# Performance work log

Hardware: AMD Instinct MI355X
Metric: run time of the kernel (lower is better)

Reference implementation:

```python
import jax, jax.numpy as jnp
import numpy as np

EMBED_DIM = 1024
NUM_HEADS = 16
HEAD_DIM = EMBED_DIM // NUM_HEADS
BATCH = 2
SEQ = 2048


def setup_inputs() -> dict:
    key = jax.random.key(0)
    ks = jax.random.split(key, 9)
    s = 1.0 / np.sqrt(EMBED_DIM)
    x = jax.random.normal(ks[0], (BATCH, SEQ, EMBED_DIM), dtype=jnp.float32)
    Wq = jax.random.uniform(ks[1], (EMBED_DIM, EMBED_DIM), jnp.float32, -s, s)
    bq = jax.random.uniform(ks[2], (EMBED_DIM,), jnp.float32, -s, s)
    Wk = jax.random.uniform(ks[3], (EMBED_DIM, EMBED_DIM), jnp.float32, -s, s)
    bk = jax.random.uniform(ks[4], (EMBED_DIM,), jnp.float32, -s, s)
    Wv = jax.random.uniform(ks[5], (EMBED_DIM, EMBED_DIM), jnp.float32, -s, s)
    bv = jax.random.uniform(ks[6], (EMBED_DIM,), jnp.float32, -s, s)
    Wo = jax.random.uniform(ks[7], (EMBED_DIM, EMBED_DIM), jnp.float32, -s, s)
    bo = jax.random.uniform(ks[8], (EMBED_DIM,), jnp.float32, -s, s)
    return {"x": x, "Wq": Wq, "bq": bq, "Wk": Wk, "bk": bk,
            "Wv": Wv, "bv": bv, "Wo": Wo, "bo": bo}


def reference(x, Wq, bq, Wk, bk, Wv, bv, Wo, bo):
    B, S, E = x.shape
    H, D = NUM_HEADS, HEAD_DIM

    def split_heads(t):
        # [B, S, E] -> [B, H, S, D]
        return t.reshape(B, S, H, D).transpose(0, 2, 1, 3)

    q = split_heads(x @ Wq + bq)
    k = split_heads(x @ Wk + bk)
    v = split_heads(x @ Wv + bv)

    scale = 1.0 / np.sqrt(D).astype(np.float32)
    scores = jnp.einsum('bhqd,bhkd->bhqk', q, k) * scale  # [B,H,S,S]
    attn = jax.nn.softmax(scores, axis=-1)
    out = jnp.einsum('bhqk,bhkd->bhqd', attn, v)  # [B,H,S,D]
    out = out.transpose(0, 2, 1, 3).reshape(B, S, E)
    return out @ Wo + bo
```

## Files before the change

### kernel.cpp

```cpp
#include <hip/hip_runtime.h>
#include <cstdint>

#define BATCH 2
#define SEQ   2048
#define EMB   1024
#define NHEAD 16
#define HDIM  64
#define NTOK  (BATCH*SEQ)

typedef __attribute__((ext_vector_type(8))) short bf16x8;
typedef __attribute__((ext_vector_type(8))) short short8;
typedef __attribute__((ext_vector_type(4))) float f32x4;

__device__ inline unsigned short f2bf(float f) {
    unsigned u = __float_as_uint(f);
    u += 0x7FFF + ((u >> 16) & 1);
    return (unsigned short)(u >> 16);
}

__device__ inline unsigned cvt_pk_bf16(float lo, float hi) {
    unsigned r;
    asm("v_cvt_pk_bf16_f32 %0, %1, %2" : "=v"(r) : "v"(lo), "v"(hi));
    return r;
}

__device__ inline void gload16(const void* g, void* lds) {
    __builtin_amdgcn_global_load_lds(
        (const __attribute__((address_space(1))) unsigned int*)g,
        (__attribute__((address_space(3))) unsigned int*)lds, 16, 0, 0);
}

__global__ __launch_bounds__(256)
void conv_x(const float* __restrict__ x, unsigned short* __restrict__ xb) {
    int i = (blockIdx.x * 256 + threadIdx.x) * 8;
    float4 a = *(const float4*)(x + i);
    float4 b = *(const float4*)(x + i + 4);
    short8 o;
    o[0]=f2bf(a.x); o[1]=f2bf(a.y); o[2]=f2bf(a.z); o[3]=f2bf(a.w);
    o[4]=f2bf(b.x); o[5]=f2bf(b.y); o[6]=f2bf(b.z); o[7]=f2bf(b.w);
    *(short8*)(xb + i) = o;
}

__global__ __launch_bounds__(256)
void conv_wt(const float* __restrict__ Wq, const float* __restrict__ Wk,
             const float* __restrict__ Wv, const float* __restrict__ Wo,
             unsigned short* __restrict__ Wt) {
    const float* W = blockIdx.z==0?Wq : blockIdx.z==1?Wk : blockIdx.z==2?Wv : Wo;
    unsigned short* out = Wt + (size_t)blockIdx.z * EMB * EMB;
    __shared__ float T[64][68];
    const int t = threadIdx.x;
    const int k0 = blockIdx.x * 64, n0 = blockIdx.y * 64;
    #pragma unroll
    for (int rr = 0; rr < 4; ++rr) {
        int row = (t >> 4) + 16 * rr;
        float4 v = *(const float4*)(W + (size_t)(k0+row)*EMB + n0 + (t&15)*4);
        *(float4*)&T[row][(t&15)*4] = v;
    }
    __syncthreads();
    #pragma unroll
    for (int it = 0; it < 2; ++it) {
        int ci = it*256 + t;
        int nr = ci >> 3, kc = ci & 7;
        short8 o;
        #pragma unroll
        for (int j = 0; j < 8; ++j) o[j] = f2bf(T[kc*8+j][nr]);
        *(short8*)(out + (size_t)(n0+nr)*EMB + k0 + kc*8) = o;
    }
}

__global__ __launch_bounds__(256)
void gemm_qkv(const unsigned short* __restrict__ xb, const unsigned short* __restrict__ Wt,
              const float* __restrict__ bq, const float* __restrict__ bk,
              const float* __restrict__ bv,
              unsigned short* __restrict__ Qb, unsigned short* __restrict__ Kb,
              unsigned short* __restrict__ Vb) {
    const int z = blockIdx.z;
    const unsigned short* W = Wt + (size_t)z * EMB * EMB;
    const float* bias = z==0 ? bq : z==1 ? bk : bv;
    unsigned short* out = z==0 ? Qb : z==1 ? Kb : Vb;
    const float scale = z==0 ? 0.125f : 1.0f;

    __shared__ __align__(16) unsigned short As[128*32];
    __shared__ __align__(16) unsigned short Bs[128*32];

    const int tid = threadIdx.x, lane = tid & 63, wid = tid >> 6;
    const int m0 = blockIdx.y * 128, n0 = blockIdx.x * 128;
    const int wr = wid >> 1, wc = wid & 1;

    f32x4 acc[4][4];
    #pragma unroll
    for (int i = 0; i < 4; ++i)
        #pragma unroll
        for (int j = 0; j < 4; ++j) acc[i][j] = f32x4{0.f,0.f,0.f,0.f};

    for (int k0 = 0; k0 < EMB; k0 += 32) {
        #pragma unroll
        for (int it = 0; it < 2; ++it) {
            int cbase = it*256 + wid*64;
            int ci = cbase + lane;
            int row = ci >> 2;
            int c = (ci & 3) ^ ((row >> 1) & 3);
            gload16(xb + (size_t)(m0+row)*EMB + k0 + c*8, (char*)As + cbase*16);
            gload16(W  + (size_t)(n0+row)*EMB + k0 + c*8, (char*)Bs + cbase*16);
        }
        __syncthreads();
        bf16x8 af[4], bf[4];
        #pragma unroll
        for (int i = 0; i < 4; ++i) {
            int ar = 64*wr + 16*i + (lane & 15);
            int ac = (lane >> 4) ^ ((ar >> 1) & 3);
            af[i] = *(const bf16x8*)((const char*)As + ar*64 + ac*16);
            int br = 64*wc + 16*i + (lane & 15);
            int bc = (lane >> 4) ^ ((br >> 1) & 3);
            bf[i] = *(const bf16x8*)((const char*)Bs + br*64 + bc*16);
        }
        #pragma unroll
        for (int i = 0; i < 4; ++i)
            #pragma unroll
            for (int j = 0; j < 4; ++j)
                acc[i][j] = __builtin_amdgcn_mfma_f32_16x16x32_bf16(af[i], bf[j], acc[i][j], 0, 0, 0);
        __syncthreads();
    }

    #pragma unroll
    for (int j = 0; j < 4; ++j) {
        int col = n0 + 64*wc + 16*j + (lane & 15);
        float bvv = bias[col];
        #pragma unroll
        for (int i = 0; i < 4; ++i) {
            int row0 = m0 + 64*wr + 16*i + (lane >> 4) * 4;
            #pragma unroll
            for (int r = 0; r < 4; ++r)
                out[(size_t)(row0+r)*EMB + col] = f2bf((acc[i][j][r] + bvv) * scale);
        }
    }
}

__global__ __launch_bounds__(256)
void gemm_out(const unsigned short* __restrict__ Cb, const unsigned short* __restrict__ Wto,
              const float* __restrict__ bo, float* __restrict__ out) {
    __shared__ __align__(16) unsigned short As[128*32];
    __shared__ __align__(16) unsigned short Bs[128*32];

    const int tid = threadIdx.x, lane = tid & 63, wid = tid >> 6;
    const int m0 = blockIdx.y * 128, n0 = blockIdx.x * 128;
    const int wr = wid >> 1, wc = wid & 1;

    f32x4 acc[4][4];
    #pragma unroll
    for (int i = 0; i < 4; ++i)
        #pragma unroll
        for (int j = 0; j < 4; ++j) acc[i][j] = f32x4{0.f,0.f,0.f,0.f};

    for (int k0 = 0; k0 < EMB; k0 += 32) {
        #pragma unroll
        for (int it = 0; it < 2; ++it) {
            int cbase = it*256 + wid*64;
            int ci = cbase + lane;
            int row = ci >> 2;
            int c = (ci & 3) ^ ((row >> 1) & 3);
            gload16(Cb  + (size_t)(m0+row)*EMB + k0 + c*8, (char*)As + cbase*16);
            gload16(Wto + (size_t)(n0+row)*EMB + k0 + c*8, (char*)Bs + cbase*16);
        }
        __syncthreads();
        bf16x8 af[4], bf[4];
        #pragma unroll
        for (int i = 0; i < 4; ++i) {
            int ar = 64*wr + 16*i + (lane & 15);
            int ac = (lane >> 4) ^ ((ar >> 1) & 3);
            af[i] = *(const bf16x8*)((const char*)As + ar*64 + ac*16);
            int br = 64*wc + 16*i + (lane & 15);
            int bc = (lane >> 4) ^ ((br >> 1) & 3);
            bf[i] = *(const bf16x8*)((const char*)Bs + br*64 + bc*16);
        }
        #pragma unroll
        for (int i = 0; i < 4; ++i)
            #pragma unroll
            for (int j = 0; j < 4; ++j)
                acc[i][j] = __builtin_amdgcn_mfma_f32_16x16x32_bf16(af[i], bf[j], acc[i][j], 0, 0, 0);
        __syncthreads();
    }

    #pragma unroll
    for (int j = 0; j < 4; ++j) {
        int col = n0 + 64*wc + 16*j + (lane & 15);
        float bvv = bo[col];
        #pragma unroll
        for (int i = 0; i < 4; ++i) {
            int row0 = m0 + 64*wr + 16*i + (lane >> 4) * 4;
            #pragma unroll
            for (int r = 0; r < 4; ++r)
                out[(size_t)(row0+r)*EMB + col] = acc[i][j][r] + bvv;
        }
    }
}

__global__ __launch_bounds__(256, 4)
void attn(const unsigned short* __restrict__ Qg, const unsigned short* __restrict__ Kg,
          const unsigned short* __restrict__ Vg, unsigned short* __restrict__ Cg) {
    __shared__ __align__(16) unsigned short Ks[2][64*64];
    __shared__ __align__(16) unsigned short Vs[2][64*64];

    const int tid = threadIdx.x, lane = tid & 63, wid = tid >> 6;
    const int qb = blockIdx.x, bh = blockIdx.y;
    const int b = bh >> 4, h = bh & 15;
    const size_t base = (size_t)b * SEQ * EMB + (size_t)h * HDIM;
    const unsigned short* Qp = Qg + base + (size_t)qb * 64 * EMB;
    const unsigned short* Kp = Kg + base;
    const unsigned short* Vp = Vg + base;

    #pragma unroll
    for (int it = 0; it < 2; ++it) {
        int ci = it*256 + tid, row = ci >> 3, c = (ci & 7) ^ (row & 7);
        gload16(Qp + (size_t)row*EMB + c*8, (char*)Ks[0] + (it*256 + wid*64)*16);
    }
    __syncthreads();
    bf16x8 qf[2];
    #pragma unroll
    for (int kc = 0; kc < 2; ++kc) {
        int r = 16*wid + (lane & 15);
        int c = ((lane >> 4) + 4*kc) ^ (r & 7);
        qf[kc] = *(const bf16x8*)((const char*)Ks[0] + r*128 + c*16);
    }
    __syncthreads();

    const int vc = tid & 7;
    const int vp = tid >> 3;

    #pragma unroll
    for (int it = 0; it < 2; ++it) {
        int ci = it*256 + tid, row = ci >> 3, c = (ci & 7) ^ (row & 7);
        gload16(Kp + (size_t)row*EMB + c*8, (char*)Ks[0] + (it*256 + wid*64)*16);
    }
    {
        short8 v0 = *(const short8*)(Vp + (size_t)(2*vp)*EMB + vc*8);
        short8 v1 = *(const short8*)(Vp + (size_t)(2*vp+1)*EMB + vc*8);
        unsigned* dst = (unsigned*)Vs[0];
        #pragma unroll
        for (int i = 0; i < 8; ++i) {
            int d = vc*8 + i;
            unsigned u = ((unsigned)(unsigned short)v1[i] << 16) | (unsigned short)v0[i];
            int slot = (vp >> 2) ^ (d & 7) ^ ((d >> 3) & 7);
            dst[d*32 + slot*4 + (vp & 3)] = u;
        }
    }
    __syncthreads();

    f32x4 O[4];
    #pragma unroll
    for (int j = 0; j < 4; ++j) O[j] = f32x4{0.f,0.f,0.f,0.f};
    float m_run = -3.0e38f, l_run = 0.f;
    const float L2E = 1.44269504f;

    for (int kt = 0; kt < SEQ/64; ++kt) {
        const int cur = kt & 1, nxt = cur ^ 1;
        short8 w0, w1;
        if (kt < SEQ/64 - 1) {
            const unsigned short* Kt = Kp + (size_t)(kt+1)*64*EMB;
            const unsigned short* Vt = Vp + (size_t)(kt+1)*64*EMB;
            #pragma unroll
            for (int it = 0; it < 2; ++it) {
                int ci = it*256 + tid, row = ci >> 3, c = (ci & 7) ^ (row & 7);
                gload16(Kt + (size_t)row*EMB + c*8, (char*)Ks[nxt] + (it*256 + wid*64)*16);
            }
            w0 = *(const short8*)(Vt + (size_t)(2*vp)*EMB + vc*8);
            w1 = *(const short8*)(Vt + (size_t)(2*vp+1)*EMB + vc*8);
        }

        f32x4 s[4];
        #pragma unroll
        for (int nk = 0; nk < 4; ++nk) {
            s[nk] = f32x4{0.f,0.f,0.f,0.f};
            #pragma unroll
            for (int kc = 0; kc < 2; ++kc) {
                int r = 16*nk + (lane & 15);
                int c = ((lane >> 4) + 4*kc) ^ (r & 7);
                bf16x8 kf = *(const bf16x8*)((const char*)Ks[cur] + r*128 + c*16);
                s[nk] = __builtin_amdgcn_mfma_f32_16x16x32_bf16(kf, qf[kc], s[nk], 0, 0, 0);
            }
        }

        float mx = s[0][0];
        #pragma unroll
        for (int nk = 0; nk < 4; ++nk)
            #pragma unroll
            for (int r = 0; r < 4; ++r) mx = fmaxf(mx, s[nk][r]);
        mx = fmaxf(mx, __shfl_xor(mx, 16));
        mx = fmaxf(mx, __shfl_xor(mx, 32));

        if (!__all(mx <= m_run + 8.0f)) {
            float mn = fmaxf(m_run, mx);
            float al = exp2f((m_run - mn) * L2E);
            m_run = mn;
            l_run *= al;
            float ar[4];
            #pragma unroll
            for (int r = 0; r < 4; ++r) ar[r] = __shfl(al, (lane >> 4)*4 + r);
            #pragma unroll
            for (int jd = 0; jd < 4; ++jd)
                #pragma unroll
                for (int r = 0; r < 4; ++r) O[jd][r] *= ar[r];
        }
        float msc = m_run * L2E;
        float ps = 0.f;
        #pragma unroll
        for (int nk = 0; nk < 4; ++nk)
            #pragma unroll
            for (int r = 0; r < 4; ++r) {
                float p = exp2f(fmaf(s[nk][r], L2E, -msc));
                s[nk][r] = p;
                ps += p;
            }
        ps += __shfl_xor(ps, 16);
        ps += __shfl_xor(ps, 32);
        l_run += ps;

        unsigned pk[4][2];
        #pragma unroll
        for (int nk = 0; nk < 4; ++nk) {
            pk[nk][0] = cvt_pk_bf16(s[nk][0], s[nk][1]);
            pk[nk][1] = cvt_pk_bf16(s[nk][2], s[nk][3]);
        }
        const int hh = lane >> 4;
        const int srcA = (((hh << 1) & 3) << 4) | (lane & 15);
        const int srcB = srcA + 16;
        const int hs = hh >> 1;
        bf16x8 pf[2];
        #pragma unroll
        for (int kc = 0; kc < 2; ++kc) {
            union { unsigned u[4]; bf16x8 v; } cvt;
            unsigned a0 = __shfl((int)pk[2*kc][0], srcA), b0 = __shfl((int)pk[2*kc+1][0], srcA);
            cvt.u[0] = hs ? b0 : a0;
            unsigned a1 = __shfl((int)pk[2*kc][1], srcA), b1 = __shfl((int)pk[2*kc+1][1], srcA);
            cvt.u[1] = hs ? b1 : a1;
            unsigned a2 = __shfl((int)pk[2*kc][0], srcB), b2 = __shfl((int)pk[2*kc+1][0], srcB);
            cvt.u[2] = hs ? b2 : a2;
            unsigned a3 = __shfl((int)pk[2*kc][1], srcB), b3 = __shfl((int)pk[2*kc+1][1], srcB);
            cvt.u[3] = hs ? b3 : a3;
            pf[kc] = cvt.v;
        }

        #pragma unroll
        for (int jd = 0; jd < 4; ++jd) {
            #pragma unroll
            for (int kc = 0; kc < 2; ++kc) {
                int d = 16*jd + (lane & 15);
                int c = ((lane >> 4) + 4*kc) ^ (d & 7) ^ ((d >> 3) & 7);
                bf16x8 vf = *(const bf16x8*)((const char*)Vs[cur] + d*128 + c*16);
                O[jd] = __builtin_amdgcn_mfma_f32_16x16x32_bf16(pf[kc], vf, O[jd], 0, 0, 0);
            }
        }

        if (kt < SEQ/64 - 1) {
            unsigned* dst = (unsigned*)Vs[nxt];
            #pragma unroll
            for (int i = 0; i < 8; ++i) {
                int d = vc*8 + i;
                unsigned u = ((unsigned)(unsigned short)w1[i] << 16) | (unsigned short)w0[i];
                int slot = (vp >> 2) ^ (d & 7) ^ ((d >> 3) & 7);
                dst[d*32 + slot*4 + (vp & 3)] = u;
            }
        }
        __syncthreads();
    }

    float inv[4];
    #pragma unroll
    for (int r = 0; r < 4; ++r) inv[r] = 1.f / __shfl(l_run, (lane >> 4)*4 + r);
    unsigned short* Cp = Cg + base + (size_t)qb * 64 * EMB;
    #pragma unroll
    for (int jd = 0; jd < 4; ++jd)
        #pragma unroll
        for (int r = 0; r < 4; ++r) {
            int row = 16*wid + (lane >> 4)*4 + r;
            int col = 16*jd + (lane & 15);
            Cp[(size_t)row*EMB + col] = f2bf(O[jd][r] * inv[r]);
        }
}

extern "C" void kernel_launch(void* const* d_in, const int* in_sizes, int n_in,
                              void* d_out, int out_size, void* d_ws, size_t ws_size,
                              hipStream_t stream) {
    const float* x  = (const float*)d_in[0];
    const float* Wq = (const float*)d_in[1];
    const float* bq = (const float*)d_in[2];
    const float* Wk = (const float*)d_in[3];
    const float* bk = (const float*)d_in[4];
    const float* Wv = (const float*)d_in[5];
    const float* bv = (const float*)d_in[6];
    const float* Wo = (const float*)d_in[7];
    const float* bo = (const float*)d_in[8];
    float* out = (float*)d_out;

    unsigned short* xb = (unsigned short*)d_ws;
    unsigned short* Wt = xb + (size_t)NTOK * EMB;
    unsigned short* Qb = Wt + (size_t)4 * EMB * EMB;
    unsigned short* Kb = Qb + (size_t)NTOK * EMB;
    unsigned short* Vb = Kb + (size_t)NTOK * EMB;
    unsigned short* Cb = Vb + (size_t)NTOK * EMB;

    conv_x<<<dim3((NTOK*EMB)/(256*8)), 256, 0, stream>>>(x, xb);
    conv_wt<<<dim3(16, 16, 4), 256, 0, stream>>>(Wq, Wk, Wv, Wo, Wt);
    gemm_qkv<<<dim3(8, 32, 3), 256, 0, stream>>>(xb, Wt, bq, bk, bv, Qb, Kb, Vb);
    attn<<<dim3(32, 32), 256, 0, stream>>>(Qb, Kb, Vb, Cb);
    gemm_out<<<dim3(8, 32), 256, 0, stream>>>(Cb, Wt + (size_t)3*EMB*EMB, bo, out);
}
```

Measured before the change: 227.8 us.

## Pre-transpose V, async-load it in attention, shrink gemm_out tile, add setprio

Adds a separate transpose_v kernel that writes V in a per-head [D, S] layout, so the attention loop can stream V tiles with asynchronous 16-byte global-to-LDS loads. This replaces the per-iteration register transpose and scattered LDS stores. gemm_out moves to 64x128 tiles to double the block count, and s_setprio is raised around the MFMA sections in all GEMM and attention loops. The max and sum reductions are also rewritten as trees. The cost is one extra kernel launch plus an extra read and write of V through global memory.

```diff
diff --git a/kernel.cpp b/kernel.cpp
--- a/kernel.cpp
+++ b/kernel.cpp
@@ -65,6 +65,35 @@
         #pragma unroll
         for (int j = 0; j < 8; ++j) o[j] = f2bf(T[kc*8+j][nr]);
         *(short8*)(out + (size_t)(n0+nr)*EMB + k0 + kc*8) = o;
+    }
+}
+
+__global__ __launch_bounds__(256)
+void transpose_v(const unsigned short* __restrict__ Vb, unsigned short* __restrict__ Vt) {
+    __shared__ unsigned short T[64*65];
+    const int t = threadIdx.x;
+    const int s0 = blockIdx.x * 64;
+    const int bh = blockIdx.y;
+    const int b = bh >> 4, h = bh & 15;
+    const unsigned short* src = Vb + ((size_t)b*SEQ + s0)*EMB + h*HDIM;
+    #pragma unroll
+    for (int it = 0; it < 2; ++it) {
+        int ci = it*256 + t;
+        int r = ci >> 3, c = ci & 7;
+        short8 v = *(const short8*)(src + (size_t)r*EMB + c*8);
+        #pragma unroll
+        for (int j = 0; j < 8; ++j) T[r*65 + c*8 + j] = (unsigned short)v[j];
+    }
+    __syncthreads();
+    unsigned short* dst = Vt + (size_t)bh * HDIM * SEQ + s0;
+    #pragma unroll
+    for (int it = 0; it < 2; ++it) {
+        int ci = it*256 + t;
+        int d = ci >> 3, c = ci & 7;
+        short8 o;
+        #pragma unroll
+        for (int j = 0; j < 8; ++j) o[j] = (short)T[(c*8 + j)*65 + d];
+        *(short8*)(dst + (size_t)d*SEQ + c*8) = o;
     }
 }
 
@@ -114,11 +143,13 @@
             int bc = (lane >> 4) ^ ((br >> 1) & 3);
             bf[i] = *(const bf16x8*)((const char*)Bs + br*64 + bc*16);
         }
+        __builtin_amdgcn_s_setprio(1);
         #pragma unroll
         for (int i = 0; i < 4; ++i)
             #pragma unroll
             for (int j = 0; j < 4; ++j)
                 acc[i][j] = __builtin_amdgcn_mfma_f32_16x16x32_bf16(af[i], bf[j], acc[i][j], 0, 0, 0);
+        __builtin_amdgcn_s_setprio(0);
         __syncthreads();
     }
 
@@ -139,45 +170,55 @@
 __global__ __launch_bounds__(256)
 void gemm_out(const unsigned short* __restrict__ Cb, const unsigned short* __restrict__ Wto,
               const float* __restrict__ bo, float* __restrict__ out) {
-    __shared__ __align__(16) unsigned short As[128*32];
+    __shared__ __align__(16) unsigned short As[64*32];
     __shared__ __align__(16) unsigned short Bs[128*32];
 
     const int tid = threadIdx.x, lane = tid & 63, wid = tid >> 6;
-    const int m0 = blockIdx.y * 128, n0 = blockIdx.x * 128;
+    const int m0 = blockIdx.y * 64, n0 = blockIdx.x * 128;
     const int wr = wid >> 1, wc = wid & 1;
 
-    f32x4 acc[4][4];
-    #pragma unroll
-    for (int i = 0; i < 4; ++i)
+    f32x4 acc[2][4];
+    #pragma unroll
+    for (int i = 0; i < 2; ++i)
         #pragma unroll
         for (int j = 0; j < 4; ++j) acc[i][j] = f32x4{0.f,0.f,0.f,0.f};
 
     for (int k0 = 0; k0 < EMB; k0 += 32) {
+        {
+            int ci = tid;
+            int row = ci >> 2;
+            int c = (ci & 3) ^ ((row >> 1) & 3);
+            gload16(Cb + (size_t)(m0+row)*EMB + k0 + c*8, (char*)As + (wid*64)*16);
+        }
         #pragma unroll
         for (int it = 0; it < 2; ++it) {
             int cbase = it*256 + wid*64;
             int ci = cbase + lane;
             int row = ci >> 2;
             int c = (ci & 3) ^ ((row >> 1) & 3);
-            gload16(Cb  + (size_t)(m0+row)*EMB + k0 + c*8, (char*)As + cbase*16);
             gload16(Wto + (size_t)(n0+row)*EMB + k0 + c*8, (char*)Bs + cbase*16);
         }
         __syncthreads();
-        bf16x8 af[4], bf[4];
-        #pragma unroll
-        for (int i = 0; i < 4; ++i) {
-            int ar = 64*wr + 16*i + (lane & 15);
+        bf16x8 af[2], bf[4];
+        #pragma unroll
+        for (int i = 0; i < 2; ++i) {
+            int ar = 32*wr + 16*i + (lane & 15);
             int ac = (lane >> 4) ^ ((ar >> 1) & 3);
             af[i] = *(const bf16x8*)((const char*)As + ar*64 + ac*16);
-            int br = 64*wc + 16*i + (lane & 15);
+        }
+        #pragma unroll
+        for (int j = 0; j < 4; ++j) {
+            int br = 64*wc + 16*j + (lane & 15);
             int bc = (lane >> 4) ^ ((br >> 1) & 3);
-            bf[i] = *(const bf16x8*)((const char*)Bs + br*64 + bc*16);
-        }
-        #pragma unroll
-        for (int i = 0; i < 4; ++i)
+            bf[j] = *(const bf16x8*)((const char*)Bs + br*64 + bc*16);
+        }
+        __builtin_amdgcn_s_setprio(1);
+        #pragma unroll
+        for (int i = 0; i < 2; ++i)
             #pragma unroll
             for (int j = 0; j < 4; ++j)
                 acc[i][j] = __builtin_amdgcn_mfma_f32_16x16x32_bf16(af[i], bf[j], acc[i][j], 0, 0, 0);
+        __builtin_amdgcn_s_setprio(0);
         __syncthreads();
     }
 
@@ -186,8 +227,8 @@
         int col = n0 + 64*wc + 16*j + (lane & 15);
         float bvv = bo[col];
         #pragma unroll
-        for (int i = 0; i < 4; ++i) {
-            int row0 = m0 + 64*wr + 16*i + (lane >> 4) * 4;
+        for (int i = 0; i < 2; ++i) {
+            int row0 = m0 + 32*wr + 16*i + (lane >> 4) * 4;
             #pragma unroll
             for (int r = 0; r < 4; ++r)
                 out[(size_t)(row0+r)*EMB + col] = acc[i][j][r] + bvv;
@@ -197,7 +238,7 @@
 
 __global__ __launch_bounds__(256, 4)
 void attn(const unsigned short* __restrict__ Qg, const unsigned short* __restrict__ Kg,
-          const unsigned short* __restrict__ Vg, unsigned short* __restrict__ Cg) {
+          const unsigned short* __restrict__ Vt, unsigned short* __restrict__ Cg) {
     __shared__ __align__(16) unsigned short Ks[2][64*64];
     __shared__ __align__(16) unsigned short Vs[2][64*64];
 
@@ -207,7 +248,7 @@
     const size_t base = (size_t)b * SEQ * EMB + (size_t)h * HDIM;
     const unsigned short* Qp = Qg + base + (size_t)qb * 64 * EMB;
     const unsigned short* Kp = Kg + base;
-    const unsigned short* Vp = Vg + base;
+    const unsigned short* Vtp = Vt + (size_t)bh * HDIM * SEQ;
 
     #pragma unroll
     for (int it = 0; it < 2; ++it) {
@@ -224,25 +265,11 @@
     }
     __syncthreads();
 
-    const int vc = tid & 7;
-    const int vp = tid >> 3;
-
     #pragma unroll
     for (int it = 0; it < 2; ++it) {
         int ci = it*256 + tid, row = ci >> 3, c = (ci & 7) ^ (row & 7);
         gload16(Kp + (size_t)row*EMB + c*8, (char*)Ks[0] + (it*256 + wid*64)*16);
-    }
-    {
-        short8 v0 = *(const short8*)(Vp + (size_t)(2*vp)*EMB + vc*8);
-        short8 v1 = *(const short8*)(Vp + (size_t)(2*vp+1)*EMB + vc*8);
-        unsigned* dst = (unsigned*)Vs[0];
-        #pragma unroll
-        for (int i = 0; i < 8; ++i) {
-            int d = vc*8 + i;
-            unsigned u = ((unsigned)(unsigned short)v1[i] << 16) | (unsigned short)v0[i];
-            int slot = (vp >> 2) ^ (d & 7) ^ ((d >> 3) & 7);
-            dst[d*32 + slot*4 + (vp & 3)] = u;
-        }
+        gload16(Vtp + (size_t)row*SEQ + c*8, (char*)Vs[0] + (it*256 + wid*64)*16);
     }
     __syncthreads();
 
@@ -254,20 +281,19 @@
 
     for (int kt = 0; kt < SEQ/64; ++kt) {
         const int cur = kt & 1, nxt = cur ^ 1;
-        short8 w0, w1;
         if (kt < SEQ/64 - 1) {
             const unsigned short* Kt = Kp + (size_t)(kt+1)*64*EMB;
-            const unsigned short* Vt = Vp + (size_t)(kt+1)*64*EMB;
+            const unsigned short* Vn = Vtp + (size_t)(kt+1)*64;
             #pragma unroll
             for (int it = 0; it < 2; ++it) {
                 int ci = it*256 + tid, row = ci >> 3, c = (ci & 7) ^ (row & 7);
                 gload16(Kt + (size_t)row*EMB + c*8, (char*)Ks[nxt] + (it*256 + wid*64)*16);
+                gload16(Vn + (size_t)row*SEQ + c*8, (char*)Vs[nxt] + (it*256 + wid*64)*16);
             }
-            w0 = *(const short8*)(Vt + (size_t)(2*vp)*EMB + vc*8);
-            w1 = *(const short8*)(Vt + (size_t)(2*vp+1)*EMB + vc*8);
         }
 
         f32x4 s[4];
+        __builtin_amdgcn_s_setprio(1);
         #pragma unroll
         for (int nk = 0; nk < 4; ++nk) {
             s[nk] = f32x4{0.f,0.f,0.f,0.f};
@@ -279,12 +305,13 @@
                 s[nk] = __builtin_amdgcn_mfma_f32_16x16x32_bf16(kf, qf[kc], s[nk], 0, 0, 0);
             }
         }
-
-        float mx = s[0][0];
-        #pragma unroll
-        for (int nk = 0; nk < 4; ++nk)
-            #pragma unroll
-            for (int r = 0; r < 4; ++r) mx = fmaxf(mx, s[nk][r]);
+        __builtin_amdgcn_s_setprio(0);
+
+        float m0_ = fmaxf(fmaxf(s[0][0], s[0][1]), fmaxf(s[0][2], s[0][3]));
+        float m1_ = fmaxf(fmaxf(s[1][0], s[1][1]), fmaxf(s[1][2], s[1][3]));
+        float m2_ = fmaxf(fmaxf(s[2][0], s[2][1]), fmaxf(s[2][2], s[2][3]));
+        float m3_ = fmaxf(fmaxf(s[3][0], s[3][1]), fmaxf(s[3][2], s[3][3]));
+        float mx = fmaxf(fmaxf(m0_, m1_), fmaxf(m2_, m3_));
         mx = fmaxf(mx, __shfl_xor(mx, 16));
         mx = fmaxf(mx, __shfl_xor(mx, 32));
 
@@ -302,15 +329,15 @@
                 for (int r = 0; r < 4; ++r) O[jd][r] *= ar[r];
         }
         float msc = m_run * L2E;
-        float ps = 0.f;
-        #pragma unroll
-        for (int nk = 0; nk < 4; ++nk)
-            #pragma unroll
-            for (int r = 0; r < 4; ++r) {
-                float p = exp2f(fmaf(s[nk][r], L2E, -msc));
-                s[nk][r] = p;
-                ps += p;
-            }
+        float psv[4];
+        #pragma unroll
+        for (int nk = 0; nk < 4; ++nk) {
+            #pragma unroll
+            for (int r = 0; r < 4; ++r)
+                s[nk][r] = exp2f(fmaf(s[nk][r], L2E, -msc));
+            psv[nk] = (s[nk][0] + s[nk][1]) + (s[nk][2] + s[nk][3]);
+        }
+        float ps = (psv[0] + psv[1]) + (psv[2] + psv[3]);
         ps += __shfl_xor(ps, 16);
         ps += __shfl_xor(ps, 32);
         l_run += ps;
@@ -340,27 +367,18 @@
             pf[kc] = cvt.v;
         }
 
+        __builtin_amdgcn_s_setprio(1);
         #pragma unroll
         for (int jd = 0; jd < 4; ++jd) {
             #pragma unroll
             for (int kc = 0; kc < 2; ++kc) {
                 int d = 16*jd + (lane & 15);
-                int c = ((lane >> 4) + 4*kc) ^ (d & 7) ^ ((d >> 3) & 7);
+                int c = ((lane >> 4) + 4*kc) ^ (d & 7);
                 bf16x8 vf = *(const bf16x8*)((const char*)Vs[cur] + d*128 + c*16);
                 O[jd] = __builtin_amdgcn_mfma_f32_16x16x32_bf16(pf[kc], vf, O[jd], 0, 0, 0);
             }
         }
-
-        if (kt < SEQ/64 - 1) {
-            unsigned* dst = (unsigned*)Vs[nxt];
-            #pragma unroll
-            for (int i = 0; i < 8; ++i) {
-                int d = vc*8 + i;
-                unsigned u = ((unsigned)(unsigned short)w1[i] << 16) | (unsigned short)w0[i];
-                int slot = (vp >> 2) ^ (d & 7) ^ ((d >> 3) & 7);
-                dst[d*32 + slot*4 + (vp & 3)] = u;
-            }
-        }
+        __builtin_amdgcn_s_setprio(0);
         __syncthreads();
     }
 
@@ -398,10 +416,12 @@
     unsigned short* Kb = Qb + (size_t)NTOK * EMB;
     unsigned short* Vb = Kb + (size_t)NTOK * EMB;
     unsigned short* Cb = Vb + (size_t)NTOK * EMB;
+    unsigned short* Vtr = Cb + (size_t)NTOK * EMB;
 
     conv_x<<<dim3((NTOK*EMB)/(256*8)), 256, 0, stream>>>(x, xb);
     conv_wt<<<dim3(16, 16, 4), 256, 0, stream>>>(Wq, Wk, Wv, Wo, Wt);
     gemm_qkv<<<dim3(8, 32, 3), 256, 0, stream>>>(xb, Wt, bq, bk, bv, Qb, Kb, Vb);
-    attn<<<dim3(32, 32), 256, 0, stream>>>(Qb, Kb, Vb, Cb);
-    gemm_out<<<dim3(8, 32), 256, 0, stream>>>(Cb, Wt + (size_t)3*EMB*EMB, bo, out);
-}
+    transpose_v<<<dim3(SEQ/64, BATCH*NHEAD), 256, 0, stream>>>(Vb, Vtr);
+    attn<<<dim3(SEQ/64, BATCH*NHEAD), 256, 0, stream>>>(Qb, Kb, Vtr, Cb);
+    gemm_out<<<dim3(EMB/128, NTOK/64), 256, 0, stream>>>(Cb, Wt + (size_t)3*EMB*EMB, bo, out);
+}
```

Result: no change. 226.8 us (-0.4%).
